# Optimization experiments

Hardware: AMD Instinct MI355X
Metric: run time of the kernel (lower is better)

## Reference

```python
import jax, jax.numpy as jnp
import numpy as np

NUM_HEADS = 8
GROUPS = 32
EPS = 1e-5


def setup_inputs() -> dict:
    key = jax.random.key(0)
    ks = jax.random.split(key, 4)
    B, C, H, W = 8, 512, 32, 32
    x = jax.random.normal(ks[0], (B, C, H, W), dtype=jnp.float32)
    gn_w = jnp.ones((C,), dtype=jnp.float32)
    gn_b = jnp.zeros((C,), dtype=jnp.float32)
    qkv_w = jax.random.normal(ks[1], (3 * C, C), dtype=jnp.float32) * (1.0 / np.sqrt(C))
    qkv_b = jnp.zeros((3 * C,), dtype=jnp.float32)
    proj_w = jax.random.normal(ks[2], (C, C), dtype=jnp.float32) * (1.0 / np.sqrt(C))
    proj_b = jnp.zeros((C,), dtype=jnp.float32)
    return {"x": x, "gn_w": gn_w, "gn_b": gn_b, "qkv_w": qkv_w,
            "qkv_b": qkv_b, "proj_w": proj_w, "proj_b": proj_b}


def reference(x, gn_w, gn_b, qkv_w, qkv_b, proj_w, proj_b):
    b, c, h, w = x.shape
    n = h * w
    hd = c // NUM_HEADS
    xf = x.reshape(b, c, n)
    # GroupNorm over (channels_per_group, HW) per sample
    xg = xf.reshape(b, GROUPS, -1)
    mu = jnp.mean(xg, axis=-1, keepdims=True)
    var = jnp.var(xg, axis=-1, keepdims=True)
    xn = ((xg - mu) * jax.lax.rsqrt(var + EPS)).reshape(b, c, n)
    xn = xn * gn_w[None, :, None] + gn_b[None, :, None]
    # 1x1 conv == channel matmul
    qkv = jnp.einsum('oc,bcn->bon', qkv_w, xn) + qkv_b[None, :, None]
    q, k, v = jnp.split(qkv, 3, axis=1)
    q = q.reshape(b, NUM_HEADS, hd, n)
    k = k.reshape(b, NUM_HEADS, hd, n)
    v = v.reshape(b, NUM_HEADS, hd, n)
    scale = hd ** 0.5
    score = jnp.einsum('bhdn,bhdm->bhnm', q, k) / scale  # [b,h,HW,HW]
    attn = jax.nn.softmax(score, axis=-1)
    out = jnp.einsum('bhnm,bhdm->bhnd', attn, v)  # [b,h,HW,hd]
    out = out.transpose(0, 1, 3, 2).reshape(b, c, n)
    out = jnp.einsum('oc,bcn->bon', proj_w, out) + proj_b[None, :, None]
    return x + out.reshape(b, c, h, w)
```

## Files before the change

kernel.cpp:

```cpp
#include <hip/hip_runtime.h>

typedef unsigned short u16;
typedef unsigned long long u64;
typedef __bf16 bf16x8 __attribute__((ext_vector_type(8)));
typedef float f32x4 __attribute__((ext_vector_type(4)));

#define NB 8
#define NC 512
#define NN 1024
#define NHEADS 8
#define HDIM 64
#define CPG 16
#define EPSV 1e-5f
#define LOG2E 1.44269504f

__device__ __forceinline__ float bf2f(u16 h) {
  union { unsigned u; float f; } v; v.u = ((unsigned)h) << 16; return v.f;
}
__device__ __forceinline__ u16 f2bf(float f) {
  union { float f; unsigned u; } v; v.f = f;
  unsigned r = v.u + 0x7fffu + ((v.u >> 16) & 1u);
  return (u16)(r >> 16);
}
__device__ __forceinline__ float h2f(u16 h) {
  unsigned s = (h >> 15) & 1u, e = (h >> 10) & 31u, m = h & 1023u;
  union { unsigned u; float f; } v;
  if (e == 0) { v.u = s << 31; return v.f + (s ? -1.f : 1.f) * (float)m * 5.9604645e-8f; }
  if (e == 31) { v.u = (s << 31) | 0x7F800000u | (m << 13); return v.f; }
  v.u = (s << 31) | ((e + 112u) << 23) | (m << 13);
  return v.f;
}
__device__ __forceinline__ u16 f2h(float f) {
  union { float f; unsigned u; } v; v.f = f;
  unsigned s = (v.u >> 16) & 0x8000u; int e = (int)((v.u >> 23) & 0xFF) - 112;
  unsigned m = v.u & 0x7FFFFFu;
  if (e <= 0) return (u16)s;
  if (e >= 31) return (u16)(s | 0x7C00u);
  u16 h = (u16)(s | (e << 10) | (m >> 13));
  unsigned rem = m & 0x1FFFu;
  if (rem > 0x1000u || (rem == 0x1000u && (h & 1u))) ++h;
  return h;
}
__device__ __forceinline__ float load_elem(const void* p, size_t i, int f) {
  if (f == 1) return bf2f(((const u16*)p)[i]);
  if (f == 2) return h2f(((const u16*)p)[i]);
  return ((const float*)p)[i];
}

__device__ __forceinline__ float exp2_fast(float x) {
  float r;
  asm("v_exp_f32 %0, %1" : "=v"(r) : "v"(x));
  return r;
}

__device__ __forceinline__ int detect_f(const u16* gw_raw) {
  int bf = 0, hf = 0;
#pragma unroll
  for (int i = 0; i < 16; ++i) {
    u16 w = gw_raw[i];
    bf += (w == 0x3F80u);
    hf += (w == 0x3C00u);
  }
  return (bf >= 12) ? 1 : (hf >= 12) ? 2 : 0;
}

__device__ __forceinline__ void cvt4(const void* raw, u16* dst, int i, int f) {
  if (f == 1) {
    *(uint2*)(dst + i) = *(const uint2*)((const u16*)raw + i);
  } else if (f == 0) {
    float4 v = *(const float4*)((const float*)raw + i);
    u16 o[4] = {f2bf(v.x), f2bf(v.y), f2bf(v.z), f2bf(v.w)};
    *(u64*)(dst + i) = *(const u64*)o;
  } else {
    u16 o[4];
#pragma unroll
    for (int k2 = 0; k2 < 4; ++k2) o[k2] = f2bf(h2f(((const u16*)raw)[i + k2]));
    *(u64*)(dst + i) = *(const u64*)o;
  }
}

__device__ __forceinline__ void gn_body(const void* x, int f,
                                        const void* gnw, const void* gnb,
                                        u16* xn, int bsrc, int bdst,
                                        int g, int t) {
  __shared__ float r1[256], r2[256];
  __shared__ alignas(16) float sxf[CPG * NN];
  __shared__ float sgw[CPG], sgb[CPG];
  u16* sx16 = (u16*)sxf;
  const size_t base = ((size_t)(bsrc * NC + g * CPG)) * NN;
  u16* dst = xn + ((size_t)(bdst * NC + g * CPG)) * NN;
  if (t < CPG) {
    sgw[t] = load_elem(gnw, (size_t)(g * CPG + t), f);
    sgb[t] = load_elem(gnb, (size_t)(g * CPG + t), f);
  }
  float s = 0.f, ss = 0.f;
  if (f == 1) {
    const u16* xb = (const u16*)x + base;
    for (int i0 = t * 8; i0 < CPG * NN; i0 += 2048) {
      uint4 dv = *(const uint4*)(xb + i0);
      *(uint4*)(sx16 + i0) = dv;
      const u16* pp = (const u16*)&dv;
#pragma unroll
      for (int j = 0; j < 8; ++j) { float v = bf2f(pp[j]); s += v; ss += v * v; }
    }
  } else if (f == 0) {
    const float* xb = (const float*)x + base;
    for (int i0 = t * 4; i0 < CPG * NN; i0 += 1024) {
      float4 v = *(const float4*)(xb + i0);
      *(float4*)(sxf + i0) = v;
      s += v.x + v.y + v.z + v.w;
      ss += v.x * v.x + v.y * v.y + v.z * v.z + v.w * v.w;
    }
  } else {
    for (int i = t; i < CPG * NN; i += 256) {
      float v = load_elem(x, base + i, f);
      sxf[i] = v;
      s += v; ss += v * v;
    }
  }
  r1[t] = s; r2[t] = ss; __syncthreads();
  for (int k = 128; k > 0; k >>= 1) {
    if (t < k) { r1[t] += r1[t + k]; r2[t] += r2[t + k]; }
    __syncthreads();
  }
  const float mu  = r1[0] * (1.f / 16384.f);
  const float var = r2[0] * (1.f / 16384.f) - mu * mu;
  const float rs  = rsqrtf(var + EPSV);
  if (f == 1) {
    for (int i0 = t * 8; i0 < CPG * NN; i0 += 2048) {
      const int cl = i0 >> 10;
      const float wsc = sgw[cl] * rs;
      const float bsc = sgb[cl] - mu * wsc;
      uint4 dv = *(const uint4*)(sx16 + i0);
      const u16* pp = (const u16*)&dv;
      u16 o[8];
#pragma unroll
      for (int j = 0; j < 8; ++j) o[j] = f2bf(bf2f(pp[j]) * wsc + bsc);
      *(uint4*)(dst + i0) = *(uint4*)o;
    }
  } else if (f == 0) {
    for (int i0 = t * 4; i0 < CPG * NN; i0 += 1024) {
      const int cl = i0 >> 10;
      const float wsc = sgw[cl] * rs;
      const float bsc = sgb[cl] - mu * wsc;
      float4 v = *(const float4*)(sxf + i0);
      u16 o[4] = {f2bf(v.x * wsc + bsc), f2bf(v.y * wsc + bsc),
                  f2bf(v.z * wsc + bsc), f2bf(v.w * wsc + bsc)};
      *(u64*)(dst + i0) = *(const u64*)o;
    }
  } else {
    for (int i = t; i < CPG * NN; i += 256) {
      const int cl = i >> 10;
      dst[i] = f2bf((sxf[i] - mu) * rs * sgw[cl] + sgb[cl]);
    }
  }
}

__global__ __launch_bounds__(256) void prep_all(const void* __restrict__ x,
                                                const void* __restrict__ gnw,
                                                const void* __restrict__ gnb,
                                                const void* __restrict__ qkvw,
                                                const void* __restrict__ qb,
                                                const void* __restrict__ projw,
                                                const void* __restrict__ pb,
                                                u16* __restrict__ wq16,
                                                u16* __restrict__ wp16,
                                                float* __restrict__ cqb,
                                                float* __restrict__ cpb,
                                                int* __restrict__ flag,
                                                u16* __restrict__ xn) {
  const int f = detect_f((const u16*)gnw);
  const int b = blockIdx.x;
  const int t = threadIdx.x;
  if (b < 768) {
    cvt4(qkvw, wq16, (b * 256 + t) * 4, f);
    return;
  }
  if (b < 1024) {
    cvt4(projw, wp16, ((b - 768) * 256 + t) * 4, f);
    return;
  }
  if (b < 1036) {
    const int i = (b - 1024) * 256 + t;
    if (i < 1536)      cqb[i] = load_elem(qb, (size_t)i, f);
    else if (i < 2048) cpb[i - 1536] = load_elem(pb, (size_t)(i - 1536), f);
    if (b == 1024 && t == 0) *flag = f;
    return;
  }
  const int idx = b - 1036;
  gn_body(x, f, gnw, gnb, xn, idx >> 5, idx >> 5, idx & 31, t);
}

__global__ __launch_bounds__(256) void gn_only(const void* __restrict__ x,
                                               const void* __restrict__ gnw,
                                               const void* __restrict__ gnb,
                                               u16* __restrict__ xn, int b0) {
  const int f = detect_f((const u16*)gnw);
  gn_body(x, f, gnw, gnb, xn, b0, 0, blockIdx.x, threadIdx.x);
}

__global__ __launch_bounds__(256) void gemm_mfma(const u16* __restrict__ A,
                                                 const u16* __restrict__ Bn,
                                                 const float* __restrict__ bias,
                                                 void* __restrict__ out,
                                                 const void* __restrict__ resid,
                                                 const int* __restrict__ flag,
                                                 int M, int K, int b0, int kmode) {
  __shared__ alignas(16) u16 sA[128 * 40];
  __shared__ alignas(16) u16 sB[128 * 40];
  const int m0 = blockIdx.x * 128;
  const int n0 = blockIdx.y * 128;
  const int bz = blockIdx.z;
  const int t = threadIdx.x;
  const int lane = t & 63, wv = t >> 6;
  const int wm = (wv >> 1) * 64, wn = (wv & 1) * 64;
  const int lr = lane & 15, quad = lane >> 4;
  const int f = *flag;

  const int ar0 = t >> 2, akc = (t & 3) * 8;
  const int ar1 = 64 + ar0;
  const int bc0 = t >> 4, bno = (t & 15) * 8;
  const int bc1 = 16 + bc0;

  f32x4 acc[4][4] = {};

  const u16* pa0 = A + (size_t)(m0 + ar0) * K + akc;
  const u16* pa1 = A + (size_t)(m0 + ar1) * K + akc;
  const u16* pb0 = Bn + ((size_t)bz * K + bc0) * NN + n0 + bno;
  const u16* pb1 = Bn + ((size_t)bz * K + bc1) * NN + n0 + bno;

  uint4 xa0 = *(const uint4*)(pa0);
  uint4 xa1 = *(const uint4*)(pa1);
  uint4 xb0 = *(const uint4*)(pb0);
  uint4 xb1 = *(const uint4*)(pb1);
  uint4 ya0 = *(const uint4*)(pa0 + 32);
  uint4 ya1 = *(const uint4*)(pa1 + 32);
  uint4 yb0 = *(const uint4*)(pb0 + (size_t)32 * NN);
  uint4 yb1 = *(const uint4*)(pb1 + (size_t)32 * NN);

#define GEMM_STAGE(ra0, ra1, rb0, rb1)                                   \
  {                                                                      \
    *(uint4*)(sA + ar0 * 40 + akc) = ra0;                                \
    *(uint4*)(sA + ar1 * 40 + akc) = ra1;                                \
    const u16* p0 = (const u16*)&rb0;                                    \
    const u16* p1 = (const u16*)&rb1;                                    \
    _Pragma("unroll")                                                    \
    for (int j = 0; j < 8; ++j) {                                        \
      const int row = bno + j;                                           \
      sB[row * 40 + (bc0 ^ (row & 24))] = p0[j];                         \
      sB[row * 40 + (bc1 ^ (row & 24))] = p1[j];                         \
    }                                                                    \
  }

#define GEMM_MFMA_BLOCK()                                                \
  {                                                                      \
    const u16* pA = sA + (wm + lr) * 40 + quad * 8;                      \
    bf16x8 af[4], bfv[4];                                                \
    _Pragma("unroll")                                                    \
    for (int i = 0; i < 4; ++i) {                                        \
      af[i] = *(const bf16x8*)(pA + i * 640);                            \
      const int rowB = wn + lr + i * 16;                                 \
      bfv[i] = *(const bf16x8*)(sB + rowB * 40 + ((quad * 8) ^ (rowB & 24))); \
    }                                                                    \
    _Pragma("unroll")                                                    \
    for (int i = 0; i < 4; ++i)                                          \
      _Pragma("unroll")                                                  \
      for (int j = 0; j < 4; ++j)                                        \
        acc[i][j] = __builtin_amdgcn_mfma_f32_16x16x32_bf16(af[i], bfv[j], acc[i][j], 0, 0, 0); \
  }

  for (int k0 = 0; k0 < K; k0 += 64) {
    __syncthreads();
    GEMM_STAGE(xa0, xa1, xb0, xb1);
    __syncthreads();
    if (k0 + 64 < K) {
      xa0 = *(const uint4*)(pa0 + k0 + 64);
      xa1 = *(const uint4*)(pa1 + k0 + 64);
      xb0 = *(const uint4*)(pb0 + (size_t)(k0 + 64) * NN);
      xb1 = *(const uint4*)(pb1 + (size_t)(k0 + 64) * NN);
    }
    GEMM_MFMA_BLOCK();
    __syncthreads();
    GEMM_STAGE(ya0, ya1, yb0, yb1);
    __syncthreads();
    if (k0 + 96 < K) {
      ya0 = *(const uint4*)(pa0 + k0 + 96);
      ya1 = *(const uint4*)(pa1 + k0 + 96);
      yb0 = *(const uint4*)(pb0 + (size_t)(k0 + 96) * NN);
      yb1 = *(const uint4*)(pb1 + (size_t)(k0 + 96) * NN);
    }
    GEMM_MFMA_BLOCK();
  }

  const bool kstore = (kmode != 0) && (m0 >= 512) && (m0 < 1024);
  if (kstore) {
    u16* kb2 = (u16*)out + ((size_t)(b0 + bz) * 1536 + 512) * NN;
#pragma unroll
    for (int i = 0; i < 4; ++i) {
      const int mb = m0 + wm + i * 16 + quad * 4;
      const int hh = (mb - 512) >> 6;
      const int d0 = (mb - 512) & 63;
      u16* hb = kb2 + (size_t)hh * NN * 64 + d0;
#pragma unroll
      for (int j = 0; j < 4; ++j) {
        const int col = n0 + wn + j * 16 + lr;
        u16 o[4];
#pragma unroll
        for (int r = 0; r < 4; ++r) o[r] = f2bf(acc[i][j][r] + bias[mb + r]);
        *(u64*)(hb + (size_t)col * 64) = *(const u64*)o;
      }
    }
    return;
  }
#pragma unroll
  for (int i = 0; i < 4; ++i) {
    const int mb = m0 + wm + i * 16 + quad * 4;
#pragma unroll
    for (int r = 0; r < 4; ++r) {
      const int mr = mb + r;
      const float bi = bias[mr];
#pragma unroll
      for (int j = 0; j < 4; ++j) {
        const int col = n0 + wn + j * 16 + lr;
        const size_t oidx = ((size_t)(b0 + bz) * M + mr) * NN + col;
        float v = acc[i][j][r] + bi;
        if (resid) {
          v += load_elem(resid, oidx, f);
          if (f == 1)      ((u16*)out)[oidx] = f2bf(v);
          else if (f == 2) ((u16*)out)[oidx] = f2h(v);
          else             ((float*)out)[oidx] = v;
        } else {
          ((u16*)out)[oidx] = f2bf(v);
        }
      }
    }
  }
}

__global__ __launch_bounds__(512) void attn_mfma(const u16* __restrict__ qkv,
                                                 u16* __restrict__ attnO) {
  __shared__ alignas(16) u16 sK[2][64 * 64];
  __shared__ alignas(16) u16 sV[2][64 * 64];

  const int L   = blockIdx.x + 8 * (blockIdx.y + 8 * blockIdx.z);
  const int xcd = L & 7;
  const int jj  = L >> 3;
  const int grp = xcd + 8 * (jj >> 3);
  const int qt  = jj & 7;
  const int h   = grp & 7;
  const int bz  = grp >> 3;

  const int n0 = qt * 128;
  const u16* qb    = qkv + ((size_t)bz * 1536 + h * HDIM) * NN;
  const u16* kbase = qkv + ((size_t)bz * 1536 + 512) * NN + (size_t)h * NN * HDIM;
  const u16* vb    = qb + (size_t)1024 * NN;
  const int t = threadIdx.x;
  const int lane = t & 63, wv = t >> 6;
  const int lr = lane & 15, quad = lane >> 4;

  const int qcol = n0 + wv * 16 + lr;
  union { u16 u[8]; bf16x8 v; } qa0, qa1;
#pragma unroll
  for (int e = 0; e < 8; ++e) {
    qa0.u[e] = qb[(size_t)(quad * 8 + e) * NN + qcol];
    qa1.u[e] = qb[(size_t)(quad * 8 + 32 + e) * NN + qcol];
  }
  const bf16x8 a0 = qa0.v;
  const bf16x8 a1 = qa1.v;

  const int km = t >> 3;
  const int kc = t & 7;
  const int ke = (km ^ (km >> 3)) & 7;
  const u16* kp = kbase + (size_t)km * 64 + kc * 8;
  const int ksd = km * 64 + ((kc ^ ke) * 8);

  const int sd  = t >> 3;
  const int smo = (t & 7) * 8;
  const u16* vp = vb + (size_t)sd * NN + smo;
  const int vs0 = sd * 64 + (smo ^ (8 * (sd & 7)));

  uint4 pk0, pv0;

  f32x4 acc_o[4] = {};
  float mrow = -1e30f, lrow = 0.f;

  pk0 = *(const uint4*)(kp);
  pv0 = *(const uint4*)(vp);
  *(uint4*)(&sK[0][ksd]) = pk0;
  *(uint4*)(&sV[0][vs0]) = pv0;
  pk0 = *(const uint4*)(kp + 4096);
  pv0 = *(const uint4*)(vp + 64);
  __syncthreads();

  for (int mt = 0; mt < 16; ++mt) {
    const int c = mt & 1;

    f32x4 p[4];
    __builtin_amdgcn_s_setprio(1);
#pragma unroll
    for (int j = 0; j < 4; ++j) {
      const int rk = j * 16 + lr;
      const u16* pKr = &sK[c][rk * 64];
      const int sw = ((rk ^ (rk >> 3)) & 7) * 8;
      bf16x8 k0 = *(const bf16x8*)(pKr + ((quad * 8) ^ sw));
      bf16x8 k1 = *(const bf16x8*)(pKr + ((quad * 8 + 32) ^ sw));
      f32x4 z = {0.f, 0.f, 0.f, 0.f};
      z = __builtin_amdgcn_mfma_f32_16x16x32_bf16(k0, a0, z, 0, 0, 0);
      z = __builtin_amdgcn_mfma_f32_16x16x32_bf16(k1, a1, z, 0, 0, 0);
      p[j] = z;
    }
    __builtin_amdgcn_s_setprio(0);

    float mx = -1e30f;
#pragma unroll
    for (int j = 0; j < 4; ++j)
#pragma unroll
      for (int r = 0; r < 4; ++r) mx = fmaxf(mx, p[j][r]);
    mx = fmaxf(mx, __shfl_xor(mx, 16));
    mx = fmaxf(mx, __shfl_xor(mx, 32));
    const float msc = mx * 0.125f;
    if (!__all(msc - mrow <= 8.f)) {
      const float mnew = fmaxf(mrow, msc);
      const float alpha = exp2_fast((mrow - mnew) * LOG2E);
      mrow = mnew;
      lrow *= alpha;
      float ar[4];
#pragma unroll
      for (int r = 0; r < 4; ++r) ar[r] = __shfl(alpha, quad * 4 + r);
#pragma unroll
      for (int j2 = 0; j2 < 4; ++j2)
#pragma unroll
        for (int r = 0; r < 4; ++r) acc_o[j2][r] *= ar[r];
    }
    const float m2 = mrow * LOG2E;
    float ls = 0.f;
#pragma unroll
    for (int j = 0; j < 4; ++j)
#pragma unroll
      for (int r = 0; r < 4; ++r) {
        const float pe = exp2_fast(fmaf(p[j][r], 0.18033688f, -m2));
        p[j][r] = pe;
        ls += pe;
      }
    ls += __shfl_xor(ls, 16);
    ls += __shfl_xor(ls, 32);
    lrow += ls;

    unsigned pa[4], pb2[4];
#pragma unroll
    for (int j = 0; j < 4; ++j) {
      asm("v_cvt_pk_bf16_f32 %0, %1, %2" : "=v"(pa[j]) : "v"(p[j][0]), "v"(p[j][1]));
      asm("v_cvt_pk_bf16_f32 %0, %1, %2" : "=v"(pb2[j]) : "v"(p[j][2]), "v"(p[j][3]));
    }

    __builtin_amdgcn_s_setprio(1);
#pragma unroll
    for (int ks = 0; ks < 2; ++ks) {
      union { unsigned u[4]; bf16x8 v; } af;
      af.u[0] = pa[2 * ks];
      af.u[1] = pb2[2 * ks];
      af.u[2] = pa[2 * ks + 1];
      af.u[3] = pb2[2 * ks + 1];
#pragma unroll
      for (int j2 = 0; j2 < 4; ++j2) {
        const int rv = j2 * 16 + lr;
        const int swv = 8 * (rv & 7);
        const u16* pVr = &sV[c][rv * 64];
        union { u64 q[2]; bf16x8 v; } bfv;
        bfv.q[0] = *(const u64*)(pVr + ((ks * 32 + 4 * quad) ^ swv));
        bfv.q[1] = *(const u64*)(pVr + ((ks * 32 + 16 + 4 * quad) ^ swv));
        acc_o[j2] = __builtin_amdgcn_mfma_f32_16x16x32_bf16(af.v, bfv.v, acc_o[j2], 0, 0, 0);
      }
    }
    __builtin_amdgcn_s_setprio(0);

    if (mt < 15) {
      const int cn = c ^ 1;
      *(uint4*)(&sK[cn][ksd]) = pk0;
      *(uint4*)(&sV[cn][vs0]) = pv0;
      if (mt < 14) {
        pk0 = *(const uint4*)(kp + (size_t)(mt + 2) * 4096);
        pv0 = *(const uint4*)(vp + (mt + 2) * 64);
      }
      __syncthreads();
    }
  }

  const float invl = 1.f / lrow;
  float ir[4];
#pragma unroll
  for (int r = 0; r < 4; ++r) ir[r] = __shfl(invl, quad * 4 + r);
  const int qrow = n0 + wv * 16 + quad * 4;
#pragma unroll
  for (int j2 = 0; j2 < 4; ++j2) {
    const int d = j2 * 16 + lr;
    u16 o[4];
#pragma unroll
    for (int r = 0; r < 4; ++r) o[r] = f2bf(acc_o[j2][r] * ir[r]);
    *(u64*)(attnO + ((size_t)bz * NC + h * HDIM + d) * NN + qrow) = *(const u64*)o;
  }
}

__global__ void sig_small_ws(u16* out) {
  if (threadIdx.x == 0 && blockIdx.x == 0) out[0] = f2bf(20000.f);
}

extern "C" void kernel_launch(void* const* d_in, const int* in_sizes, int n_in,
                              void* d_out, int out_size, void* d_ws, size_t ws_size,
                              hipStream_t stream) {
  const void* x      = d_in[0];
  const void* gn_w   = d_in[1];
  const void* gn_b   = d_in[2];
  const void* qkv_w  = d_in[3];
  const void* qkv_b  = d_in[4];
  const void* proj_w = d_in[5];
  const void* proj_b = d_in[6];
  char* ws = (char*)d_ws;
  const size_t MB = (size_t)1 << 20;

  u16*   wq16 = (u16*)(ws);
  u16*   wp16 = (u16*)(ws + 3 * MB / 2);
  float* cqb  = (float*)(ws + 2 * MB);
  float* cpb  = (float*)(ws + 2 * MB + 8192);
  int*   flag = (int*)  (ws + 2 * MB + 16384);

  if (ws_size >= 36 * MB) {
    u16* xn    = (u16*)(ws + 3 * MB);
    u16* qkvb  = (u16*)(ws + 11 * MB);
    u16* attnO = xn;
    prep_all<<<dim3(1036 + NB * 32), dim3(256), 0, stream>>>(
        x, gn_w, gn_b, qkv_w, qkv_b, proj_w, proj_b,
        wq16, wp16, cqb, cpb, flag, xn);
    gemm_mfma<<<dim3(12, 8, NB), dim3(256), 0, stream>>>(wq16, xn, cqb, qkvb,
                                                         nullptr, flag, 1536, NC, 0, 1);
    attn_mfma<<<dim3(8, NHEADS, NB), dim3(512), 0, stream>>>(qkvb, attnO);
    gemm_mfma<<<dim3(4, 8, NB), dim3(256), 0, stream>>>(wp16, attnO, cpb, d_out,
                                                        x, flag, NC, NC, 0, 0);
  } else if (ws_size >= 9 * MB) {
    u16* xn    = (u16*)(ws + 3 * MB);
    u16* qkvb  = (u16*)(ws + 4 * MB);
    u16* attnO = (u16*)(ws + 7 * MB);
    prep_all<<<dim3(1036), dim3(256), 0, stream>>>(
        x, gn_w, gn_b, qkv_w, qkv_b, proj_w, proj_b,
        wq16, wp16, cqb, cpb, flag, xn);
    for (int b = 0; b < NB; ++b) {
      gn_only<<<dim3(32), dim3(256), 0, stream>>>(x, gn_w, gn_b, xn, b);
      gemm_mfma<<<dim3(12, 8, 1), dim3(256), 0, stream>>>(wq16, xn, cqb, qkvb,
                                                          nullptr, flag, 1536, NC, 0, 1);
      attn_mfma<<<dim3(8, NHEADS, 1), dim3(512), 0, stream>>>(qkvb, attnO);
      gemm_mfma<<<dim3(4, 8, 1), dim3(256), 0, stream>>>(wp16, attnO, cpb, d_out,
                                                         x, flag, NC, NC, b, 0);
    }
  } else {
    sig_small_ws<<<dim3(1), dim3(64), 0, stream>>>((u16*)d_out);
  }
}
```

Before: 184.8 us.

## Store GEMM B operands token-major to vectorize shared-memory staging

The GroupNorm output and the attention output are now written transposed, as [batch, token, channel]. The GEMM B tile can then be loaded with contiguous 16-byte reads along K and stored to LDS with a single swizzled vector write, replacing the per-element scattered LDS stores. The cost is that GroupNorm writes become strided 32-byte chunks per token and attention writes become scalar 2-byte stores with stride NC, which may hurt write coalescing. GroupNorm also now stages its input as fp32 in LDS for the bf16 path.

```diff
diff --git a/kernel.cpp b/kernel.cpp
--- a/kernel.cpp
+++ b/kernel.cpp
@@ -81,14 +81,12 @@
 
 __device__ __forceinline__ void gn_body(const void* x, int f,
                                         const void* gnw, const void* gnb,
-                                        u16* xn, int bsrc, int bdst,
+                                        u16* xnT, int bsrc, int bdst,
                                         int g, int t) {
   __shared__ float r1[256], r2[256];
   __shared__ alignas(16) float sxf[CPG * NN];
   __shared__ float sgw[CPG], sgb[CPG];
-  u16* sx16 = (u16*)sxf;
   const size_t base = ((size_t)(bsrc * NC + g * CPG)) * NN;
-  u16* dst = xn + ((size_t)(bdst * NC + g * CPG)) * NN;
   if (t < CPG) {
     sgw[t] = load_elem(gnw, (size_t)(g * CPG + t), f);
     sgb[t] = load_elem(gnb, (size_t)(g * CPG + t), f);
@@ -98,10 +96,12 @@
     const u16* xb = (const u16*)x + base;
     for (int i0 = t * 8; i0 < CPG * NN; i0 += 2048) {
       uint4 dv = *(const uint4*)(xb + i0);
-      *(uint4*)(sx16 + i0) = dv;
       const u16* pp = (const u16*)&dv;
-#pragma unroll
-      for (int j = 0; j < 8; ++j) { float v = bf2f(pp[j]); s += v; ss += v * v; }
+      float vv[8];
+#pragma unroll
+      for (int j = 0; j < 8; ++j) { vv[j] = bf2f(pp[j]); s += vv[j]; ss += vv[j] * vv[j]; }
+      *(float4*)(sxf + i0)     = make_float4(vv[0], vv[1], vv[2], vv[3]);
+      *(float4*)(sxf + i0 + 4) = make_float4(vv[4], vv[5], vv[6], vv[7]);
     }
   } else if (f == 0) {
     const float* xb = (const float*)x + base;
@@ -126,33 +126,21 @@
   const float mu  = r1[0] * (1.f / 16384.f);
   const float var = r2[0] * (1.f / 16384.f) - mu * mu;
   const float rs  = rsqrtf(var + EPSV);
-  if (f == 1) {
-    for (int i0 = t * 8; i0 < CPG * NN; i0 += 2048) {
-      const int cl = i0 >> 10;
-      const float wsc = sgw[cl] * rs;
-      const float bsc = sgb[cl] - mu * wsc;
-      uint4 dv = *(const uint4*)(sx16 + i0);
-      const u16* pp = (const u16*)&dv;
-      u16 o[8];
-#pragma unroll
-      for (int j = 0; j < 8; ++j) o[j] = f2bf(bf2f(pp[j]) * wsc + bsc);
-      *(uint4*)(dst + i0) = *(uint4*)o;
-    }
-  } else if (f == 0) {
-    for (int i0 = t * 4; i0 < CPG * NN; i0 += 1024) {
-      const int cl = i0 >> 10;
-      const float wsc = sgw[cl] * rs;
-      const float bsc = sgb[cl] - mu * wsc;
-      float4 v = *(const float4*)(sxf + i0);
-      u16 o[4] = {f2bf(v.x * wsc + bsc), f2bf(v.y * wsc + bsc),
-                  f2bf(v.z * wsc + bsc), f2bf(v.w * wsc + bsc)};
-      *(u64*)(dst + i0) = *(const u64*)o;
-    }
-  } else {
-    for (int i = t; i < CPG * NN; i += 256) {
-      const int cl = i >> 10;
-      dst[i] = f2bf((sxf[i] - mu) * rs * sgw[cl] + sgb[cl]);
-    }
+  float wsc[CPG], bsc[CPG];
+#pragma unroll
+  for (int cl = 0; cl < CPG; ++cl) {
+    wsc[cl] = sgw[cl] * rs;
+    bsc[cl] = sgb[cl] - mu * wsc[cl];
+  }
+  u16* dstb = xnT + (size_t)bdst * NN * NC + g * CPG;
+  for (int n = t; n < NN; n += 256) {
+    u16 o[CPG];
+#pragma unroll
+    for (int cl = 0; cl < CPG; ++cl)
+      o[cl] = f2bf(sxf[cl * NN + n] * wsc[cl] + bsc[cl]);
+    u16* dr = dstb + (size_t)n * NC;
+    *(uint4*)(dr)     = *(const uint4*)(o);
+    *(uint4*)(dr + 8) = *(const uint4*)(o + 8);
   }
 }
 
@@ -168,7 +156,7 @@
                                                 float* __restrict__ cqb,
                                                 float* __restrict__ cpb,
                                                 int* __restrict__ flag,
-                                                u16* __restrict__ xn) {
+                                                u16* __restrict__ xnT) {
   const int f = detect_f((const u16*)gnw);
   const int b = blockIdx.x;
   const int t = threadIdx.x;
@@ -188,19 +176,19 @@
     return;
   }
   const int idx = b - 1036;
-  gn_body(x, f, gnw, gnb, xn, idx >> 5, idx >> 5, idx & 31, t);
+  gn_body(x, f, gnw, gnb, xnT, idx >> 5, idx >> 5, idx & 31, t);
 }
 
 __global__ __launch_bounds__(256) void gn_only(const void* __restrict__ x,
                                                const void* __restrict__ gnw,
                                                const void* __restrict__ gnb,
-                                               u16* __restrict__ xn, int b0) {
+                                               u16* __restrict__ xnT, int b0) {
   const int f = detect_f((const u16*)gnw);
-  gn_body(x, f, gnw, gnb, xn, b0, 0, blockIdx.x, threadIdx.x);
+  gn_body(x, f, gnw, gnb, xnT, b0, 0, blockIdx.x, threadIdx.x);
 }
 
 __global__ __launch_bounds__(256) void gemm_mfma(const u16* __restrict__ A,
-                                                 const u16* __restrict__ Bn,
+                                                 const u16* __restrict__ BnT,
                                                  const float* __restrict__ bias,
                                                  void* __restrict__ out,
                                                  const void* __restrict__ resid,
@@ -219,15 +207,15 @@
 
   const int ar0 = t >> 2, akc = (t & 3) * 8;
   const int ar1 = 64 + ar0;
-  const int bc0 = t >> 4, bno = (t & 15) * 8;
-  const int bc1 = 16 + bc0;
+  const int sw0 = akc ^ (ar0 & 24);
+  const int sw1 = akc ^ (ar1 & 24);
 
   f32x4 acc[4][4] = {};
 
   const u16* pa0 = A + (size_t)(m0 + ar0) * K + akc;
   const u16* pa1 = A + (size_t)(m0 + ar1) * K + akc;
-  const u16* pb0 = Bn + ((size_t)bz * K + bc0) * NN + n0 + bno;
-  const u16* pb1 = Bn + ((size_t)bz * K + bc1) * NN + n0 + bno;
+  const u16* pb0 = BnT + ((size_t)bz * NN + n0 + ar0) * K + akc;
+  const u16* pb1 = BnT + ((size_t)bz * NN + n0 + ar1) * K + akc;
 
   uint4 xa0 = *(const uint4*)(pa0);
   uint4 xa1 = *(const uint4*)(pa1);
@@ -235,21 +223,15 @@
   uint4 xb1 = *(const uint4*)(pb1);
   uint4 ya0 = *(const uint4*)(pa0 + 32);
   uint4 ya1 = *(const uint4*)(pa1 + 32);
-  uint4 yb0 = *(const uint4*)(pb0 + (size_t)32 * NN);
-  uint4 yb1 = *(const uint4*)(pb1 + (size_t)32 * NN);
+  uint4 yb0 = *(const uint4*)(pb0 + 32);
+  uint4 yb1 = *(const uint4*)(pb1 + 32);
 
 #define GEMM_STAGE(ra0, ra1, rb0, rb1)                                   \
   {                                                                      \
     *(uint4*)(sA + ar0 * 40 + akc) = ra0;                                \
     *(uint4*)(sA + ar1 * 40 + akc) = ra1;                                \
-    const u16* p0 = (const u16*)&rb0;                                    \
-    const u16* p1 = (const u16*)&rb1;                                    \
-    _Pragma("unroll")                                                    \
-    for (int j = 0; j < 8; ++j) {                                        \
-      const int row = bno + j;                                           \
-      sB[row * 40 + (bc0 ^ (row & 24))] = p0[j];                         \
-      sB[row * 40 + (bc1 ^ (row & 24))] = p1[j];                         \
-    }                                                                    \
+    *(uint4*)(sB + ar0 * 40 + sw0) = rb0;                                \
+    *(uint4*)(sB + ar1 * 40 + sw1) = rb1;                                \
   }
 
 #define GEMM_MFMA_BLOCK()                                                \
@@ -276,8 +258,8 @@
     if (k0 + 64 < K) {
       xa0 = *(const uint4*)(pa0 + k0 + 64);
       xa1 = *(const uint4*)(pa1 + k0 + 64);
-      xb0 = *(const uint4*)(pb0 + (size_t)(k0 + 64) * NN);
-      xb1 = *(const uint4*)(pb1 + (size_t)(k0 + 64) * NN);
+      xb0 = *(const uint4*)(pb0 + k0 + 64);
+      xb1 = *(const uint4*)(pb1 + k0 + 64);
     }
     GEMM_MFMA_BLOCK();
     __syncthreads();
@@ -286,8 +268,8 @@
     if (k0 + 96 < K) {
       ya0 = *(const uint4*)(pa0 + k0 + 96);
       ya1 = *(const uint4*)(pa1 + k0 + 96);
-      yb0 = *(const uint4*)(pb0 + (size_t)(k0 + 96) * NN);
-      yb1 = *(const uint4*)(pb1 + (size_t)(k0 + 96) * NN);
+      yb0 = *(const uint4*)(pb0 + k0 + 96);
+      yb1 = *(const uint4*)(pb1 + k0 + 96);
     }
     GEMM_MFMA_BLOCK();
   }
@@ -338,7 +320,7 @@
 }
 
 __global__ __launch_bounds__(512) void attn_mfma(const u16* __restrict__ qkv,
-                                                 u16* __restrict__ attnO) {
+                                                 u16* __restrict__ attnOT) {
   __shared__ alignas(16) u16 sK[2][64 * 64];
   __shared__ alignas(16) u16 sV[2][64 * 64];
 
@@ -492,12 +474,11 @@
   for (int r = 0; r < 4; ++r) ir[r] = __shfl(invl, quad * 4 + r);
   const int qrow = n0 + wv * 16 + quad * 4;
 #pragma unroll
-  for (int j2 = 0; j2 < 4; ++j2) {
-    const int d = j2 * 16 + lr;
-    u16 o[4];
-#pragma unroll
-    for (int r = 0; r < 4; ++r) o[r] = f2bf(acc_o[j2][r] * ir[r]);
-    *(u64*)(attnO + ((size_t)bz * NC + h * HDIM + d) * NN + qrow) = *(const u64*)o;
+  for (int r = 0; r < 4; ++r) {
+    u16* orow = attnOT + ((size_t)bz * NN + qrow + r) * NC + h * HDIM;
+#pragma unroll
+    for (int j2 = 0; j2 < 4; ++j2)
+      orow[j2 * 16 + lr] = f2bf(acc_o[j2][r] * ir[r]);
   }
 }
 
@@ -525,30 +506,30 @@
   int*   flag = (int*)  (ws + 2 * MB + 16384);
 
   if (ws_size >= 36 * MB) {
-    u16* xn    = (u16*)(ws + 3 * MB);
-    u16* qkvb  = (u16*)(ws + 11 * MB);
-    u16* attnO = xn;
+    u16* xnT    = (u16*)(ws + 3 * MB);
+    u16* qkvb   = (u16*)(ws + 11 * MB);
+    u16* attnOT = xnT;
     prep_all<<<dim3(1036 + NB * 32), dim3(256), 0, stream>>>(
         x, gn_w, gn_b, qkv_w, qkv_b, proj_w, proj_b,
-        wq16, wp16, cqb, cpb, flag, xn);
-    gemm_mfma<<<dim3(12, 8, NB), dim3(256), 0, stream>>>(wq16, xn, cqb, qkvb,
+        wq16, wp16, cqb, cpb, flag, xnT);
+    gemm_mfma<<<dim3(12, 8, NB), dim3(256), 0, stream>>>(wq16, xnT, cqb, qkvb,
                                                          nullptr, flag, 1536, NC, 0, 1);
-    attn_mfma<<<dim3(8, NHEADS, NB), dim3(512), 0, stream>>>(qkvb, attnO);
-    gemm_mfma<<<dim3(4, 8, NB), dim3(256), 0, stream>>>(wp16, attnO, cpb, d_out,
+    attn_mfma<<<dim3(8, NHEADS, NB), dim3(512), 0, stream>>>(qkvb, attnOT);
+    gemm_mfma<<<dim3(4, 8, NB), dim3(256), 0, stream>>>(wp16, attnOT, cpb, d_out,
                                                         x, flag, NC, NC, 0, 0);
   } else if (ws_size >= 9 * MB) {
-    u16* xn    = (u16*)(ws + 3 * MB);
-    u16* qkvb  = (u16*)(ws + 4 * MB);
-    u16* attnO = (u16*)(ws + 7 * MB);
+    u16* xnT    = (u16*)(ws + 3 * MB);
+    u16* qkvb   = (u16*)(ws + 4 * MB);
+    u16* attnOT = (u16*)(ws + 7 * MB);
     prep_all<<<dim3(1036), dim3(256), 0, stream>>>(
         x, gn_w, gn_b, qkv_w, qkv_b, proj_w, proj_b,
-        wq16, wp16, cqb, cpb, flag, xn);
+        wq16, wp16, cqb, cpb, flag, xnT);
     for (int b = 0; b < NB; ++b) {
-      gn_only<<<dim3(32), dim3(256), 0, stream>>>(x, gn_w, gn_b, xn, b);
-      gemm_mfma<<<dim3(12, 8, 1), dim3(256), 0, stream>>>(wq16, xn, cqb, qkvb,
+      gn_only<<<dim3(32), dim3(256), 0, stream>>>(x, gn_w, gn_b, xnT, b);
+      gemm_mfma<<<dim3(12, 8, 1), dim3(256), 0, stream>>>(wq16, xnT, cqb, qkvb,
                                                           nullptr, flag, 1536, NC, 0, 1);
-      attn_mfma<<<dim3(8, NHEADS, 1), dim3(512), 0, stream>>>(qkvb, attnO);
-      gemm_mfma<<<dim3(4, 8, 1), dim3(256), 0, stream>>>(wp16, attnO, cpb, d_out,
+      attn_mfma<<<dim3(8, NHEADS, 1), dim3(512), 0, stream>>>(qkvb, attnOT);
+      gemm_mfma<<<dim3(4, 8, 1), dim3(256), 0, stream>>>(wp16, attnOT, cpb, d_out,
                                                          x, flag, NC, NC, b, 0);
     }
   } else {
```

Measured after the change: 178.6 us. 3.3% less time.
